# Performance work log

Hardware: AMD Instinct MI355X
Metric: run time of the kernel (lower is better)

## Reference

```python
import jax, jax.numpy as jnp
import numpy as np

N_NODES = 50000
N_EDGES = 800000
NODE_DIM = 256
EDGE_DIM = 64
HIDDEN = 256
LN_EPS = 1e-5


def setup_inputs() -> dict:
    key = jax.random.key(0)
    ks = jax.random.split(key, 12)
    s = 0.05
    return {
        "edge_attr": jax.random.normal(ks[0], (N_EDGES, EDGE_DIM), jnp.float32),
        "node_attr": jax.random.normal(ks[1], (N_NODES, NODE_DIM), jnp.float32),
        "edge_index": jax.random.randint(ks[2], (2, N_EDGES), 0, N_NODES, jnp.int64),
        # split first linear: [hidden, edge_dim], [hidden, node_dim], [hidden, node_dim]
        "edge_lin": jax.random.normal(ks[3], (HIDDEN, EDGE_DIM), jnp.float32) * s,
        "src_lin": jax.random.normal(ks[4], (HIDDEN, NODE_DIM), jnp.float32) * s,
        "dst_lin": jax.random.normal(ks[5], (HIDDEN, NODE_DIM), jnp.float32) * s,
        "bias": jax.random.normal(ks[6], (HIDDEN,), jnp.float32) * s,
        # mlp: ReLU -> Linear(hidden,hidden) -> ReLU -> Linear(hidden,edge_dim) -> LayerNorm
        "W1": jax.random.normal(ks[7], (HIDDEN, HIDDEN), jnp.float32) * s,
        "b1": jax.random.normal(ks[8], (HIDDEN,), jnp.float32) * s,
        "W2": jax.random.normal(ks[9], (EDGE_DIM, HIDDEN), jnp.float32) * s,
        "b2": jax.random.normal(ks[10], (EDGE_DIM,), jnp.float32) * s,
        "ln_gamma": jnp.ones((EDGE_DIM,), jnp.float32),
        "ln_beta": jnp.zeros((EDGE_DIM,), jnp.float32),
    }


def reference(edge_attr, node_attr, edge_index, edge_lin, src_lin, dst_lin,
              bias, W1, b1, W2, b2, ln_gamma, ln_beta):
    # pre-project nodes once, then gather per-edge (sum trick)
    mlp_edge = edge_attr @ edge_lin.T                 # [E, H]
    mlp_src = node_attr @ src_lin.T                   # [N, H]
    mlp_dst = node_attr @ dst_lin.T + bias            # [N, H]
    src, dst = edge_index[0], edge_index[1]
    h = mlp_edge + mlp_src[src] + mlp_dst[dst]        # [E, H]
    # MLP: ReLU -> Linear -> ReLU -> Linear -> LayerNorm
    h = jax.nn.relu(h)
    h = jax.nn.relu(h @ W1.T + b1)                    # [E, H]
    y = h @ W2.T + b2                                 # [E, edge_dim]
    mu = jnp.mean(y, axis=-1, keepdims=True)
    var = jnp.mean(jnp.square(y - mu), axis=-1, keepdims=True)
    y = (y - mu) * jax.lax.rsqrt(var + LN_EPS) * ln_gamma + ln_beta
    return y
```

## Files before the change

### kernel.cpp

```cpp
#include <hip/hip_runtime.h>
#include <stdint.h>

#define EN 800000
#define NN 50000
#define HID 256
#define ED 64
#define LN_EPS 1e-5f

typedef __attribute__((ext_vector_type(8))) short bf8_t;
typedef __attribute__((ext_vector_type(4))) float f32x4;

union BF8 { unsigned short u[8]; bf8_t v; };

__device__ __forceinline__ unsigned short f2bf(float f) {
  union { float f; uint32_t u; } x; x.f = f;
  return (unsigned short)((x.u + 0x7FFFu + ((x.u >> 16) & 1u)) >> 16);
}
__device__ __forceinline__ float bf2f(uint32_t h) {
  union { uint32_t u; float f; } x; x.u = h << 16;
  return x.f;
}
__device__ __forceinline__ bf8_t pack8(float4 f0, float4 f1) {
  BF8 u;
  u.u[0] = f2bf(f0.x); u.u[1] = f2bf(f0.y); u.u[2] = f2bf(f0.z); u.u[3] = f2bf(f0.w);
  u.u[4] = f2bf(f1.x); u.u[5] = f2bf(f1.y); u.u[6] = f2bf(f1.z); u.u[7] = f2bf(f1.w);
  return u.v;
}

#define MFMA(a, b, c) __builtin_amdgcn_mfma_f32_16x16x32_bf16((a), (b), (c), 0, 0, 0)

__global__ void k_cvt_w(const float* __restrict__ W1, const float* __restrict__ W2,
                        const float* __restrict__ EL,
                        unsigned short* __restrict__ W1b, unsigned short* __restrict__ W2b,
                        unsigned short* __restrict__ ELb) {
  int i = blockIdx.x * blockDim.x + threadIdx.x;
  int stride = blockDim.x * gridDim.x;
  for (int j = i; j < HID * HID; j += stride) W1b[j] = f2bf(W1[j]);
  for (int j = i; j < ED * HID; j += stride) W2b[j] = f2bf(W2[j]);
  for (int j = i; j < HID * ED; j += stride) ELb[j] = f2bf(EL[j]);
}

__launch_bounds__(256)
__global__ void k_node_proj(const float* __restrict__ node_attr,
                            const float* __restrict__ src_lin,
                            const float* __restrict__ dst_lin,
                            const float* __restrict__ bias,
                            unsigned short* __restrict__ Psrc,
                            unsigned short* __restrict__ Pdst) {
  __shared__ __align__(16) char s_a[64 * 512];
  const int tid = threadIdx.x;
  const int wid = tid >> 6;
  const int lane = tid & 63;
  const int l16 = lane & 15, lq = lane >> 4;
  const int m0 = blockIdx.x * 64;

  for (int c = tid; c < 64 * 32; c += 256) {
    int row = c >> 5, kc = c & 31;
    int grow = m0 + row;
    bf8_t val;
    if (grow < NN) {
      const float4* p = (const float4*)(node_attr + grow * HID + kc * 8);
      val = pack8(p[0], p[1]);
    } else {
      BF8 z;
      #pragma unroll
      for (int j = 0; j < 8; ++j) z.u[j] = 0;
      val = z.v;
    }
    *(bf8_t*)(s_a + row * 512 + ((kc ^ (row & 7)) << 4)) = val;
  }
  __syncthreads();

  const int n0 = wid * 64;
  for (int pass = 0; pass < 2; ++pass) {
    const float* W = pass ? dst_lin : src_lin;
    f32x4 acc[4][4] = {};
    #pragma unroll
    for (int ks = 0; ks < 8; ++ks) {
      bf8_t a[4], b[4];
      #pragma unroll
      for (int mi = 0; mi < 4; ++mi) {
        int row = mi * 16 + l16;
        a[mi] = *(const bf8_t*)(s_a + row * 512 + (((ks * 4 + lq) ^ (row & 7)) << 4));
      }
      #pragma unroll
      for (int ni = 0; ni < 4; ++ni) {
        const float4* p = (const float4*)(W + (n0 + ni * 16 + l16) * HID + ks * 32 + lq * 8);
        b[ni] = pack8(p[0], p[1]);
      }
      #pragma unroll
      for (int mi = 0; mi < 4; ++mi)
        #pragma unroll
        for (int ni = 0; ni < 4; ++ni)
          acc[mi][ni] = MFMA(a[mi], b[ni], acc[mi][ni]);
    }
    unsigned short* P = pass ? Pdst : Psrc;
    #pragma unroll
    for (int ni = 0; ni < 4; ++ni) {
      int col = n0 + ni * 16 + l16;
      float bia = pass ? bias[col] : 0.f;
      #pragma unroll
      for (int mi = 0; mi < 4; ++mi) {
        #pragma unroll
        for (int r = 0; r < 4; ++r) {
          int row = m0 + mi * 16 + lq * 4 + r;
          if (row < NN) P[row * HID + col] = f2bf(acc[mi][ni][r] + bia);
        }
      }
    }
  }
}

__launch_bounds__(256)
__global__ void k_edge_main(const float* __restrict__ edge_attr,
                            const int* __restrict__ edge_index,
                            const unsigned short* __restrict__ Psrc,
                            const unsigned short* __restrict__ Pdst,
                            const unsigned short* __restrict__ ELb,
                            const unsigned short* __restrict__ W1b,
                            const unsigned short* __restrict__ W2b,
                            const float* __restrict__ b1,
                            const float* __restrict__ b2,
                            const float* __restrict__ gam,
                            const float* __restrict__ bet,
                            float* __restrict__ out) {
  __shared__ __align__(16) char s_h[64 * 512];
  __shared__ __align__(16) char s_e[64 * 128];
  __shared__ int s_src[64], s_dst[64];

  const int tid = threadIdx.x;
  const int wid = tid >> 6;
  const int lane = tid & 63;
  const int l16 = lane & 15, lq = lane >> 4;
  const int e0 = blockIdx.x * 64;

  if (tid < 64) s_src[tid] = edge_index[e0 + tid];
  else if (tid < 128) s_dst[tid - 64] = edge_index[EN + e0 + (tid - 64)];

  #pragma unroll
  for (int i = 0; i < 2; ++i) {
    int c = tid + i * 256;
    int row = c >> 3, kc = c & 7;
    const float4* p = (const float4*)(edge_attr + (e0 + row) * ED + kc * 8);
    *(bf8_t*)(s_e + row * 128 + ((kc ^ (row & 7)) << 4)) = pack8(p[0], p[1]);
  }
  __syncthreads();

  #pragma unroll 4
  for (int i = 0; i < 16; ++i) {
    int er = wid * 16 + i;
    int s = s_src[er], d = s_dst[er];
    const uint2* ps = (const uint2*)(Psrc + s * HID) + lane;
    const uint2* pd = (const uint2*)(Pdst + d * HID) + lane;
    uint2 a = *ps, b = *pd;
    float v0 = bf2f(a.x & 0xffffu) + bf2f(b.x & 0xffffu);
    float v1 = bf2f(a.x >> 16)     + bf2f(b.x >> 16);
    float v2 = bf2f(a.y & 0xffffu) + bf2f(b.y & 0xffffu);
    float v3 = bf2f(a.y >> 16)     + bf2f(b.y >> 16);
    uint2 o;
    o.x = (uint32_t)f2bf(v0) | ((uint32_t)f2bf(v1) << 16);
    o.y = (uint32_t)f2bf(v2) | ((uint32_t)f2bf(v3) << 16);
    int chunk = lane >> 1;
    *(uint2*)(s_h + er * 512 + ((chunk ^ (er & 7)) << 4) + ((lane & 1) << 3)) = o;
  }

  const int n0 = wid * 64;
  f32x4 acc[4][4] = {};
  #pragma unroll
  for (int ks = 0; ks < 2; ++ks) {
    bf8_t a[4], b[4];
    #pragma unroll
    for (int mi = 0; mi < 4; ++mi) {
      int row = mi * 16 + l16;
      a[mi] = *(const bf8_t*)(s_e + row * 128 + (((ks * 4 + lq) ^ (row & 7)) << 4));
    }
    #pragma unroll
    for (int ni = 0; ni < 4; ++ni)
      b[ni] = *(const bf8_t*)(ELb + (n0 + ni * 16 + l16) * ED + ks * 32 + lq * 8);
    #pragma unroll
    for (int mi = 0; mi < 4; ++mi)
      #pragma unroll
      for (int ni = 0; ni < 4; ++ni)
        acc[mi][ni] = MFMA(a[mi], b[ni], acc[mi][ni]);
  }
  __syncthreads();

  #pragma unroll
  for (int mi = 0; mi < 4; ++mi) {
    #pragma unroll
    for (int ni = 0; ni < 4; ++ni) {
      int col = n0 + ni * 16 + l16;
      #pragma unroll
      for (int r = 0; r < 4; ++r) {
        int row = mi * 16 + lq * 4 + r;
        unsigned short* p = (unsigned short*)(s_h + row * 512 +
                              (((col >> 3) ^ (row & 7)) << 4) + ((col & 7) << 1));
        float v = acc[mi][ni][r] + bf2f(*p);
        *p = f2bf(fmaxf(v, 0.f));
      }
    }
  }
  __syncthreads();

  #pragma unroll
  for (int mi = 0; mi < 4; ++mi)
    #pragma unroll
    for (int ni = 0; ni < 4; ++ni)
      acc[mi][ni] = (f32x4){0.f, 0.f, 0.f, 0.f};
  #pragma unroll
  for (int ks = 0; ks < 8; ++ks) {
    bf8_t a[4], b[4];
    #pragma unroll
    for (int mi = 0; mi < 4; ++mi) {
      int row = mi * 16 + l16;
      a[mi] = *(const bf8_t*)(s_h + row * 512 + (((ks * 4 + lq) ^ (row & 7)) << 4));
    }
    #pragma unroll
    for (int ni = 0; ni < 4; ++ni)
      b[ni] = *(const bf8_t*)(W1b + (n0 + ni * 16 + l16) * HID + ks * 32 + lq * 8);
    #pragma unroll
    for (int mi = 0; mi < 4; ++mi)
      #pragma unroll
      for (int ni = 0; ni < 4; ++ni)
        acc[mi][ni] = MFMA(a[mi], b[ni], acc[mi][ni]);
  }
  __syncthreads();

  #pragma unroll
  for (int ni = 0; ni < 4; ++ni) {
    int col = n0 + ni * 16 + l16;
    float bia = b1[col];
    #pragma unroll
    for (int mi = 0; mi < 4; ++mi) {
      #pragma unroll
      for (int r = 0; r < 4; ++r) {
        int row = mi * 16 + lq * 4 + r;
        *(unsigned short*)(s_h + row * 512 +
            (((col >> 3) ^ (row & 7)) << 4) + ((col & 7) << 1))
            = f2bf(fmaxf(acc[mi][ni][r] + bia, 0.f));
      }
    }
  }
  __syncthreads();

  f32x4 acc3[4] = {};
  #pragma unroll
  for (int ks = 0; ks < 8; ++ks) {
    int row = wid * 16 + l16;
    bf8_t a = *(const bf8_t*)(s_h + row * 512 + (((ks * 4 + lq) ^ (row & 7)) << 4));
    #pragma unroll
    for (int ni = 0; ni < 4; ++ni) {
      bf8_t b = *(const bf8_t*)(W2b + (ni * 16 + l16) * HID + ks * 32 + lq * 8);
      acc3[ni] = MFMA(a, b, acc3[ni]);
    }
  }

  float vals[4][4];
  float sum[4] = {0.f, 0.f, 0.f, 0.f}, ssq[4] = {0.f, 0.f, 0.f, 0.f};
  #pragma unroll
  for (int ni = 0; ni < 4; ++ni) {
    int col = ni * 16 + l16;
    float bia = b2[col];
    #pragma unroll
    for (int r = 0; r < 4; ++r) {
      float v = acc3[ni][r] + bia;
      vals[ni][r] = v;
      sum[r] += v;
      ssq[r] += v * v;
    }
  }
  #pragma unroll
  for (int m = 1; m < 16; m <<= 1) {
    #pragma unroll
    for (int r = 0; r < 4; ++r) {
      sum[r] += __shfl_xor(sum[r], m, 64);
      ssq[r] += __shfl_xor(ssq[r], m, 64);
    }
  }
  float mu[4], rstd[4];
  #pragma unroll
  for (int r = 0; r < 4; ++r) {
    mu[r] = sum[r] * (1.f / 64.f);
    float var = ssq[r] * (1.f / 64.f) - mu[r] * mu[r];
    rstd[r] = rsqrtf(var + LN_EPS);
  }
  #pragma unroll
  for (int ni = 0; ni < 4; ++ni) {
    int col = ni * 16 + l16;
    float g = gam[col], be = bet[col];
    #pragma unroll
    for (int r = 0; r < 4; ++r) {
      int row = e0 + wid * 16 + lq * 4 + r;
      out[row * ED + col] = (vals[ni][r] - mu[r]) * rstd[r] * g + be;
    }
  }
}

extern "C" void kernel_launch(void* const* d_in, const int* in_sizes, int n_in,
                              void* d_out, int out_size, void* d_ws, size_t ws_size,
                              hipStream_t stream) {
  const float* edge_attr = (const float*)d_in[0];
  const float* node_attr = (const float*)d_in[1];
  const int* edge_index = (const int*)d_in[2];
  const float* edge_lin = (const float*)d_in[3];
  const float* src_lin = (const float*)d_in[4];
  const float* dst_lin = (const float*)d_in[5];
  const float* bias = (const float*)d_in[6];
  const float* W1 = (const float*)d_in[7];
  const float* b1 = (const float*)d_in[8];
  const float* W2 = (const float*)d_in[9];
  const float* b2 = (const float*)d_in[10];
  const float* gam = (const float*)d_in[11];
  const float* bet = (const float*)d_in[12];
  float* out = (float*)d_out;

  char* ws = (char*)d_ws;
  unsigned short* Psrc = (unsigned short*)(ws + 0);
  unsigned short* Pdst = (unsigned short*)(ws + 25600000);
  unsigned short* W1b = (unsigned short*)(ws + 51200000);
  unsigned short* W2b = (unsigned short*)(ws + 51331072);
  unsigned short* ELb = (unsigned short*)(ws + 51363840);

  hipLaunchKernelGGL(k_cvt_w, dim3(128), dim3(256), 0, stream,
                     W1, W2, edge_lin, W1b, W2b, ELb);
  hipLaunchKernelGGL(k_node_proj, dim3((NN + 63) / 64), dim3(256), 0, stream,
                     node_attr, src_lin, dst_lin, bias, Psrc, Pdst);
  hipLaunchKernelGGL(k_edge_main, dim3(EN / 64), dim3(256), 0, stream,
                     edge_attr, edge_index, Psrc, Pdst, ELb, W1b, W2b,
                     b1, b2, gam, bet, out);
}
```

Baseline: 740.7 us.

## Split edge kernel into gather+first-GEMM and MLP kernels via workspace buffer

Splits the fused per-edge kernel in two. The first kernel gathers the node projections, adds the edge projection, applies ReLU and writes a bf16 hidden buffer to workspace. The second kernel reads that buffer directly from global memory for the W1 and W2 GEMMs and the LayerNorm, and both kernels use launch bounds requesting 3 blocks per CU to raise occupancy. The cost is an extra write and read of about 400MB of intermediates, with work chunked to fit the workspace, and the old fused kernel is kept as a fallback when the workspace is too small.

```diff
diff --git a/kernel.cpp b/kernel.cpp
--- a/kernel.cpp
+++ b/kernel.cpp
@@ -59,7 +59,7 @@
     int grow = m0 + row;
     bf8_t val;
     if (grow < NN) {
-      const float4* p = (const float4*)(node_attr + grow * HID + kc * 8);
+      const float4* p = (const float4*)(node_attr + (size_t)grow * HID + kc * 8);
       val = pack8(p[0], p[1]);
     } else {
       BF8 z;
@@ -85,7 +85,7 @@
       }
       #pragma unroll
       for (int ni = 0; ni < 4; ++ni) {
-        const float4* p = (const float4*)(W + (n0 + ni * 16 + l16) * HID + ks * 32 + lq * 8);
+        const float4* p = (const float4*)(W + (size_t)(n0 + ni * 16 + l16) * HID + ks * 32 + lq * 8);
         b[ni] = pack8(p[0], p[1]);
       }
       #pragma unroll
@@ -104,26 +104,21 @@
         #pragma unroll
         for (int r = 0; r < 4; ++r) {
           int row = m0 + mi * 16 + lq * 4 + r;
-          if (row < NN) P[row * HID + col] = f2bf(acc[mi][ni][r] + bia);
+          if (row < NN) P[(size_t)row * HID + col] = f2bf(acc[mi][ni][r] + bia);
         }
       }
     }
   }
 }
 
-__launch_bounds__(256)
-__global__ void k_edge_main(const float* __restrict__ edge_attr,
+__launch_bounds__(256, 3)
+__global__ void k_gather_g1(const float* __restrict__ edge_attr,
                             const int* __restrict__ edge_index,
                             const unsigned short* __restrict__ Psrc,
                             const unsigned short* __restrict__ Pdst,
                             const unsigned short* __restrict__ ELb,
-                            const unsigned short* __restrict__ W1b,
-                            const unsigned short* __restrict__ W2b,
-                            const float* __restrict__ b1,
-                            const float* __restrict__ b2,
-                            const float* __restrict__ gam,
-                            const float* __restrict__ bet,
-                            float* __restrict__ out) {
+                            unsigned short* __restrict__ H0,
+                            int chunk_base) {
   __shared__ __align__(16) char s_h[64 * 512];
   __shared__ __align__(16) char s_e[64 * 128];
   __shared__ int s_src[64], s_dst[64];
@@ -132,7 +127,9 @@
   const int wid = tid >> 6;
   const int lane = tid & 63;
   const int l16 = lane & 15, lq = lane >> 4;
-  const int e0 = blockIdx.x * 64;
+  const int e0 = chunk_base + blockIdx.x * 64;
+  const int h0 = blockIdx.x * 64;
+  const int n0 = wid * 64;
 
   if (tid < 64) s_src[tid] = edge_index[e0 + tid];
   else if (tid < 128) s_dst[tid - 64] = edge_index[EN + e0 + (tid - 64)];
@@ -141,7 +138,7 @@
   for (int i = 0; i < 2; ++i) {
     int c = tid + i * 256;
     int row = c >> 3, kc = c & 7;
-    const float4* p = (const float4*)(edge_attr + (e0 + row) * ED + kc * 8);
+    const float4* p = (const float4*)(edge_attr + (size_t)(e0 + row) * ED + kc * 8);
     *(bf8_t*)(s_e + row * 128 + ((kc ^ (row & 7)) << 4)) = pack8(p[0], p[1]);
   }
   __syncthreads();
@@ -150,8 +147,8 @@
   for (int i = 0; i < 16; ++i) {
     int er = wid * 16 + i;
     int s = s_src[er], d = s_dst[er];
-    const uint2* ps = (const uint2*)(Psrc + s * HID) + lane;
-    const uint2* pd = (const uint2*)(Pdst + d * HID) + lane;
+    const uint2* ps = (const uint2*)(Psrc + (size_t)s * HID) + lane;
+    const uint2* pd = (const uint2*)(Pdst + (size_t)d * HID) + lane;
     uint2 a = *ps, b = *pd;
     float v0 = bf2f(a.x & 0xffffu) + bf2f(b.x & 0xffffu);
     float v1 = bf2f(a.x >> 16)     + bf2f(b.x >> 16);
@@ -164,7 +161,6 @@
     *(uint2*)(s_h + er * 512 + ((chunk ^ (er & 7)) << 4) + ((lane & 1) << 3)) = o;
   }
 
-  const int n0 = wid * 64;
   f32x4 acc[4][4] = {};
   #pragma unroll
   for (int ks = 0; ks < 2; ++ks) {
@@ -203,28 +199,50 @@
   __syncthreads();
 
   #pragma unroll
-  for (int mi = 0; mi < 4; ++mi)
-    #pragma unroll
-    for (int ni = 0; ni < 4; ++ni)
-      acc[mi][ni] = (f32x4){0.f, 0.f, 0.f, 0.f};
+  for (int i = 0; i < 8; ++i) {
+    int c = tid + i * 256;
+    int row = c >> 5, kc = c & 31;
+    bf8_t val = *(const bf8_t*)(s_h + row * 512 + ((kc ^ (row & 7)) << 4));
+    *(bf8_t*)(H0 + ((size_t)(h0 + row) << 8) + kc * 8) = val;
+  }
+}
+
+__launch_bounds__(256, 3)
+__global__ void k_mlp(const unsigned short* __restrict__ H0,
+                      const unsigned short* __restrict__ W1b,
+                      const unsigned short* __restrict__ W2b,
+                      const float* __restrict__ b1,
+                      const float* __restrict__ b2,
+                      const float* __restrict__ gam,
+                      const float* __restrict__ bet,
+                      float* __restrict__ out,
+                      int chunk_base) {
+  __shared__ __align__(16) char s_h[64 * 512];
+
+  const int tid = threadIdx.x;
+  const int wid = tid >> 6;
+  const int lane = tid & 63;
+  const int l16 = lane & 15, lq = lane >> 4;
+  const int eloc = blockIdx.x * 64;
+  const int eglob = chunk_base + eloc;
+  const int n0 = wid * 64;
+
+  f32x4 acc[4][4] = {};
   #pragma unroll
   for (int ks = 0; ks < 8; ++ks) {
     bf8_t a[4], b[4];
     #pragma unroll
-    for (int mi = 0; mi < 4; ++mi) {
-      int row = mi * 16 + l16;
-      a[mi] = *(const bf8_t*)(s_h + row * 512 + (((ks * 4 + lq) ^ (row & 7)) << 4));
-    }
+    for (int mi = 0; mi < 4; ++mi)
+      a[mi] = *(const bf8_t*)(H0 + ((size_t)(eloc + mi * 16 + l16) << 8) + ks * 32 + lq * 8);
     #pragma unroll
     for (int ni = 0; ni < 4; ++ni)
-      b[ni] = *(const bf8_t*)(W1b + (n0 + ni * 16 + l16) * HID + ks * 32 + lq * 8);
+      b[ni] = *(const bf8_t*)(W1b + (size_t)(n0 + ni * 16 + l16) * HID + ks * 32 + lq * 8);
     #pragma unroll
     for (int mi = 0; mi < 4; ++mi)
       #pragma unroll
       for (int ni = 0; ni < 4; ++ni)
         acc[mi][ni] = MFMA(a[mi], b[ni], acc[mi][ni]);
   }
-  __syncthreads();
 
   #pragma unroll
   for (int ni = 0; ni < 4; ++ni) {
@@ -290,11 +308,198 @@
     float g = gam[col], be = bet[col];
     #pragma unroll
     for (int r = 0; r < 4; ++r) {
+      int row = eglob + wid * 16 + lq * 4 + r;
+      out[(size_t)row * ED + col] = (vals[ni][r] - mu[r]) * rstd[r] * g + be;
+    }
+  }
+}
+
+__launch_bounds__(256)
+__global__ void k_edge_fused(const float* __restrict__ edge_attr,
+                             const int* __restrict__ edge_index,
+                             const unsigned short* __restrict__ Psrc,
+                             const unsigned short* __restrict__ Pdst,
+                             const unsigned short* __restrict__ ELb,
+                             const unsigned short* __restrict__ W1b,
+                             const unsigned short* __restrict__ W2b,
+                             const float* __restrict__ b1,
+                             const float* __restrict__ b2,
+                             const float* __restrict__ gam,
+                             const float* __restrict__ bet,
+                             float* __restrict__ out) {
+  __shared__ __align__(16) char s_h[64 * 512];
+  __shared__ __align__(16) char s_e[64 * 128];
+  __shared__ int s_src[64], s_dst[64];
+
+  const int tid = threadIdx.x;
+  const int wid = tid >> 6;
+  const int lane = tid & 63;
+  const int l16 = lane & 15, lq = lane >> 4;
+  const int e0 = blockIdx.x * 64;
+
+  if (tid < 64) s_src[tid] = edge_index[e0 + tid];
+  else if (tid < 128) s_dst[tid - 64] = edge_index[EN + e0 + (tid - 64)];
+
+  #pragma unroll
+  for (int i = 0; i < 2; ++i) {
+    int c = tid + i * 256;
+    int row = c >> 3, kc = c & 7;
+    const float4* p = (const float4*)(edge_attr + (size_t)(e0 + row) * ED + kc * 8);
+    *(bf8_t*)(s_e + row * 128 + ((kc ^ (row & 7)) << 4)) = pack8(p[0], p[1]);
+  }
+  __syncthreads();
+
+  #pragma unroll 4
+  for (int i = 0; i < 16; ++i) {
+    int er = wid * 16 + i;
+    int s = s_src[er], d = s_dst[er];
+    const uint2* ps = (const uint2*)(Psrc + (size_t)s * HID) + lane;
+    const uint2* pd = (const uint2*)(Pdst + (size_t)d * HID) + lane;
+    uint2 a = *ps, b = *pd;
+    float v0 = bf2f(a.x & 0xffffu) + bf2f(b.x & 0xffffu);
+    float v1 = bf2f(a.x >> 16)     + bf2f(b.x >> 16);
+    float v2 = bf2f(a.y & 0xffffu) + bf2f(b.y & 0xffffu);
+    float v3 = bf2f(a.y >> 16)     + bf2f(b.y >> 16);
+    uint2 o;
+    o.x = (uint32_t)f2bf(v0) | ((uint32_t)f2bf(v1) << 16);
+    o.y = (uint32_t)f2bf(v2) | ((uint32_t)f2bf(v3) << 16);
+    int chunk = lane >> 1;
+    *(uint2*)(s_h + er * 512 + ((chunk ^ (er & 7)) << 4) + ((lane & 1) << 3)) = o;
+  }
+
+  const int n0 = wid * 64;
+  f32x4 acc[4][4] = {};
+  #pragma unroll
+  for (int ks = 0; ks < 2; ++ks) {
+    bf8_t a[4], b[4];
+    #pragma unroll
+    for (int mi = 0; mi < 4; ++mi) {
+      int row = mi * 16 + l16;
+      a[mi] = *(const bf8_t*)(s_e + row * 128 + (((ks * 4 + lq) ^ (row & 7)) << 4));
+    }
+    #pragma unroll
+    for (int ni = 0; ni < 4; ++ni)
+      b[ni] = *(const bf8_t*)(ELb + (n0 + ni * 16 + l16) * ED + ks * 32 + lq * 8);
+    #pragma unroll
+    for (int mi = 0; mi < 4; ++mi)
+      #pragma unroll
+      for (int ni = 0; ni < 4; ++ni)
+        acc[mi][ni] = MFMA(a[mi], b[ni], acc[mi][ni]);
+  }
+  __syncthreads();
+
+  #pragma unroll
+  for (int mi = 0; mi < 4; ++mi) {
+    #pragma unroll
+    for (int ni = 0; ni < 4; ++ni) {
+      int col = n0 + ni * 16 + l16;
+      #pragma unroll
+      for (int r = 0; r < 4; ++r) {
+        int row = mi * 16 + lq * 4 + r;
+        unsigned short* p = (unsigned short*)(s_h + row * 512 +
+                              (((col >> 3) ^ (row & 7)) << 4) + ((col & 7) << 1));
+        float v = acc[mi][ni][r] + bf2f(*p);
+        *p = f2bf(fmaxf(v, 0.f));
+      }
+    }
+  }
+  __syncthreads();
+
+  #pragma unroll
+  for (int mi = 0; mi < 4; ++mi)
+    #pragma unroll
+    for (int ni = 0; ni < 4; ++ni)
+      acc[mi][ni] = (f32x4){0.f, 0.f, 0.f, 0.f};
+  #pragma unroll
+  for (int ks = 0; ks < 8; ++ks) {
+    bf8_t a[4], b[4];
+    #pragma unroll
+    for (int mi = 0; mi < 4; ++mi) {
+      int row = mi * 16 + l16;
+      a[mi] = *(const bf8_t*)(s_h + row * 512 + (((ks * 4 + lq) ^ (row & 7)) << 4));
+    }
+    #pragma unroll
+    for (int ni = 0; ni < 4; ++ni)
+      b[ni] = *(const bf8_t*)(W1b + (size_t)(n0 + ni * 16 + l16) * HID + ks * 32 + lq * 8);
+    #pragma unroll
+    for (int mi = 0; mi < 4; ++mi)
+      #pragma unroll
+      for (int ni = 0; ni < 4; ++ni)
+        acc[mi][ni] = MFMA(a[mi], b[ni], acc[mi][ni]);
+  }
+  __syncthreads();
+
+  #pragma unroll
+  for (int ni = 0; ni < 4; ++ni) {
+    int col = n0 + ni * 16 + l16;
+    float bia = b1[col];
+    #pragma unroll
+    for (int mi = 0; mi < 4; ++mi) {
+      #pragma unroll
+      for (int r = 0; r < 4; ++r) {
+        int row = mi * 16 + lq * 4 + r;
+        *(unsigned short*)(s_h + row * 512 +
+            (((col >> 3) ^ (row & 7)) << 4) + ((col & 7) << 1))
+            = f2bf(fmaxf(acc[mi][ni][r] + bia, 0.f));
+      }
+    }
+  }
+  __syncthreads();
+
+  f32x4 acc3[4] = {};
+  #pragma unroll
+  for (int ks = 0; ks < 8; ++ks) {
+    int row = wid * 16 + l16;
+    bf8_t a = *(const bf8_t*)(s_h + row * 512 + (((ks * 4 + lq) ^ (row & 7)) << 4));
+    #pragma unroll
+    for (int ni = 0; ni < 4; ++ni) {
+      bf8_t b = *(const bf8_t*)(W2b + (ni * 16 + l16) * HID + ks * 32 + lq * 8);
+      acc3[ni] = MFMA(a, b, acc3[ni]);
+    }
+  }
+
+  float vals[4][4];
+  float sum[4] = {0.f, 0.f, 0.f, 0.f}, ssq[4] = {0.f, 0.f, 0.f, 0.f};
+  #pragma unroll
+  for (int ni = 0; ni < 4; ++ni) {
+    int col = ni * 16 + l16;
+    float bia = b2[col];
+    #pragma unroll
+    for (int r = 0; r < 4; ++r) {
+      float v = acc3[ni][r] + bia;
+      vals[ni][r] = v;
+      sum[r] += v;
+      ssq[r] += v * v;
+    }
+  }
+  #pragma unroll
+  for (int m = 1; m < 16; m <<= 1) {
+    #pragma unroll
+    for (int r = 0; r < 4; ++r) {
+      sum[r] += __shfl_xor(sum[r], m, 64);
+      ssq[r] += __shfl_xor(ssq[r], m, 64);
+    }
+  }
+  float mu[4], rstd[4];
+  #pragma unroll
+  for (int r = 0; r < 4; ++r) {
+    mu[r] = sum[r] * (1.f / 64.f);
+    float var = ssq[r] * (1.f / 64.f) - mu[r] * mu[r];
+    rstd[r] = rsqrtf(var + LN_EPS);
+  }
+  #pragma unroll
+  for (int ni = 0; ni < 4; ++ni) {
+    int col = ni * 16 + l16;
+    float g = gam[col], be = bet[col];
+    #pragma unroll
+    for (int r = 0; r < 4; ++r) {
       int row = e0 + wid * 16 + lq * 4 + r;
-      out[row * ED + col] = (vals[ni][r] - mu[r]) * rstd[r] * g + be;
-    }
-  }
-}
+      out[(size_t)row * ED + col] = (vals[ni][r] - mu[r]) * rstd[r] * g + be;
+    }
+  }
+}
+
+#define TAB_END 51396608ull
 
 extern "C" void kernel_launch(void* const* d_in, const int* in_sizes, int n_in,
                               void* d_out, int out_size, void* d_ws, size_t ws_size,
@@ -317,15 +522,32 @@
   char* ws = (char*)d_ws;
   unsigned short* Psrc = (unsigned short*)(ws + 0);
   unsigned short* Pdst = (unsigned short*)(ws + 25600000);
-  unsigned short* W1b = (unsigned short*)(ws + 51200000);
-  unsigned short* W2b = (unsigned short*)(ws + 51331072);
-  unsigned short* ELb = (unsigned short*)(ws + 51363840);
+  unsigned short* W1b  = (unsigned short*)(ws + 51200000);
+  unsigned short* W2b  = (unsigned short*)(ws + 51331072);
+  unsigned short* ELb  = (unsigned short*)(ws + 51363840);
+  unsigned short* H0   = (unsigned short*)(ws + TAB_END);
 
   hipLaunchKernelGGL(k_cvt_w, dim3(128), dim3(256), 0, stream,
                      W1, W2, edge_lin, W1b, W2b, ELb);
   hipLaunchKernelGGL(k_node_proj, dim3((NN + 63) / 64), dim3(256), 0, stream,
                      node_attr, src_lin, dst_lin, bias, Psrc, Pdst);
-  hipLaunchKernelGGL(k_edge_main, dim3(EN / 64), dim3(256), 0, stream,
-                     edge_attr, edge_index, Psrc, Pdst, ELb, W1b, W2b,
-                     b1, b2, gam, bet, out);
-}
+
+  long long avail = (ws_size > TAB_END) ? (long long)(ws_size - TAB_END) : 0;
+  long long chunk = (avail / 512) / 64 * 64;
+  if (chunk > EN) chunk = EN;
+
+  if (chunk >= 64) {
+    for (long long base = 0; base < EN; base += chunk) {
+      long long cnt = EN - base < chunk ? EN - base : chunk;
+      int cblk = (int)(cnt / 64);
+      hipLaunchKernelGGL(k_gather_g1, dim3(cblk), dim3(256), 0, stream,
+                         edge_attr, edge_index, Psrc, Pdst, ELb, H0, (int)base);
+      hipLaunchKernelGGL(k_mlp, dim3(cblk), dim3(256), 0, stream,
+                         H0, W1b, W2b, b1, b2, gam, bet, out, (int)base);
+    }
+  } else {
+    hipLaunchKernelGGL(k_edge_fused, dim3(EN / 64), dim3(256), 0, stream,
+                       edge_attr, edge_index, Psrc, Pdst, ELb, W1b, W2b,
+                       b1, b2, gam, bet, out);
+  }
+}
```

Result: slower. 989.4 us (+33.6%).
